# Optimization experiments

Measured on AMD Instinct MI355X. Metric: run time of the kernel, lower is better.

The kernel has to match this reference:

```python
import jax, jax.numpy as jnp
import numpy as np

N_HEADS = 16
ROPE_BASE = 10000.0


def setup_inputs() -> dict:
    key = jax.random.key(0)
    k1, k2, k3 = jax.random.split(key, 3)
    B, S, E = 8, 1024, 128
    sequence = jax.random.normal(k1, (B, S, E), dtype=jnp.float32)
    W_qkv = jax.random.normal(k2, (3 * N_HEADS * E, E), dtype=jnp.float32) * (E ** -0.5)
    b_qkv = jax.random.normal(k3, (3 * N_HEADS * E,), dtype=jnp.float32) * 0.02
    return {"sequence": sequence, "W_qkv": W_qkv, "b_qkv": b_qkv}


def _rope(x):
    # x: [B, H, S, D]; rotate-half (NeoX style) rotary encoding
    D = x.shape[-1]
    S = x.shape[-2]
    half = D // 2
    inv_freq = 1.0 / (ROPE_BASE ** (jnp.arange(0, half, dtype=jnp.float32) / half))
    angles = jnp.arange(S, dtype=jnp.float32)[:, None] * inv_freq[None, :]  # [S, half]
    cos = jnp.cos(angles)
    sin = jnp.sin(angles)
    x1, x2 = x[..., :half], x[..., half:]
    return jnp.concatenate([x1 * cos - x2 * sin, x1 * sin + x2 * cos], axis=-1)


def reference(sequence, W_qkv, b_qkv):
    B, S, E = sequence.shape
    H = N_HEADS
    # fused QKV projection: [B, S, 3*H*E]
    qkv = jnp.einsum('bse,fe->bsf', sequence, W_qkv) + b_qkv
    qkv = qkv.reshape(B, S, 3, H, E)
    # split and move head dim: [B, H, S, E]
    q = jnp.transpose(qkv[:, :, 0], (0, 2, 1, 3))
    k = jnp.transpose(qkv[:, :, 1], (0, 2, 1, 3))
    v = jnp.transpose(qkv[:, :, 2], (0, 2, 1, 3))
    q = _rope(q)
    k = _rope(k)
    # scaled dot-product attention (non-causal, dropout_p=0 for input layer)
    scale = 1.0 / jnp.sqrt(jnp.asarray(E, dtype=q.dtype))
    scores = jnp.einsum('bhqd,bhkd->bhqk', q, k) * scale
    probs = jax.nn.softmax(scores, axis=-1)
    attn = jnp.einsum('bhqk,bhkd->bhqd', probs, v)
    # back to [B, S, H, E]
    return jnp.transpose(attn, (0, 2, 1, 3))
```

## Files before the change

kernel.cpp:

```cpp
#include <hip/hip_runtime.h>
#include <hip/hip_bf16.h>
#include <math.h>

typedef __attribute__((ext_vector_type(8))) short bf16x8;
typedef __attribute__((ext_vector_type(4))) float f32x4;
typedef __attribute__((ext_vector_type(16))) float f32x16;

#define B_ 8
#define S_ 1024
#define E_ 128
#define H_ 16
#define M_ (B_*S_)
#define F_ (3*H_*E_)

__device__ __forceinline__ unsigned short f2b(float x) {
  __hip_bfloat16 h = __float2bfloat16(x);
  return *reinterpret_cast<unsigned short*>(&h);
}

__device__ __forceinline__ f32x4 mfma16(bf16x8 a, bf16x8 b, f32x4 c) {
  return __builtin_amdgcn_mfma_f32_16x16x32_bf16(a, b, c, 0, 0, 0);
}
__device__ __forceinline__ f32x16 mfma32(bf16x8 a, bf16x8 b, f32x16 c) {
  return __builtin_amdgcn_mfma_f32_32x32x16_bf16(a, b, c, 0, 0, 0);
}
__device__ __forceinline__ unsigned cvtpk(float a, float b) {
  unsigned r; asm("v_cvt_pk_bf16_f32 %0, %1, %2" : "=v"(r) : "v"(a), "v"(b)); return r;
}

__global__ __launch_bounds__(256) void prep_kernel(
    const float* __restrict__ seq, const float* __restrict__ wq,
    unsigned short* __restrict__ seqb, unsigned short* __restrict__ wb,
    float* __restrict__ ctab, float* __restrict__ stab)
{
  int i = blockIdx.x * 256 + threadIdx.x;
  if (i < M_*E_/4) {
    float4 v = reinterpret_cast<const float4*>(seq)[i];
    ushort4 o; o.x = f2b(v.x); o.y = f2b(v.y); o.z = f2b(v.z); o.w = f2b(v.w);
    reinterpret_cast<ushort4*>(seqb)[i] = o;
  }
  if (i < F_*E_/4) {
    float4 v = reinterpret_cast<const float4*>(wq)[i];
    ushort4 o; o.x = f2b(v.x); o.y = f2b(v.y); o.z = f2b(v.z); o.w = f2b(v.w);
    reinterpret_cast<ushort4*>(wb)[i] = o;
  }
  if (i < S_*64) {
    int s = i >> 6, e = i & 63;
    double ang = (double)s * pow(10000.0, -(double)e / 64.0);
    ctab[i] = (float)cos(ang);
    stab[i] = (float)sin(ang);
  }
}

__global__ __launch_bounds__(256) void qkv_gemm_kernel(
    const unsigned short* __restrict__ Ab, const unsigned short* __restrict__ Wb,
    const float* __restrict__ bias, const float* __restrict__ ctab, const float* __restrict__ stab,
    unsigned short* __restrict__ qo, unsigned short* __restrict__ ko, unsigned short* __restrict__ vt)
{
  __shared__ unsigned short As[128][136];
  __shared__ unsigned short Ws[128][136];
  const int bm = blockIdx.x, bn = blockIdx.y;
  const int t = threadIdx.x;
  const int w = t >> 6, l = t & 63, lc = l & 15, g = l >> 4;

  #pragma unroll
  for (int i = 0; i < 8; ++i) {
    int c = t + i * 256, row = c >> 4, kc = c & 15;
    *reinterpret_cast<bf16x8*>(&As[row][kc*8]) =
        *reinterpret_cast<const bf16x8*>(&Ab[(size_t)(bm*128+row)*128 + kc*8]);
    *reinterpret_cast<bf16x8*>(&Ws[row][kc*8]) =
        *reinterpret_cast<const bf16x8*>(&Wb[(size_t)(bn*128+row)*128 + kc*8]);
  }
  __syncthreads();

  const f32x4 zero = {0.f, 0.f, 0.f, 0.f};
  f32x4 acc[2][8];
  #pragma unroll
  for (int mi=0;mi<2;mi++)
    #pragma unroll
    for (int nj=0;nj<8;nj++) acc[mi][nj] = zero;

  #pragma unroll
  for (int ks = 0; ks < 4; ++ks) {
    bf16x8 a[2], b[8];
    #pragma unroll
    for (int mi=0;mi<2;mi++)
      a[mi] = *reinterpret_cast<const bf16x8*>(&As[w*32 + mi*16 + lc][ks*32 + g*8]);
    #pragma unroll
    for (int nj=0;nj<8;nj++)
      b[nj] = *reinterpret_cast<const bf16x8*>(&Ws[nj*16 + lc][ks*32 + g*8]);
    #pragma unroll
    for (int mi=0;mi<2;mi++)
      #pragma unroll
      for (int nj=0;nj<8;nj++)
        acc[mi][nj] = mfma16(a[mi], b[nj], acc[mi][nj]);
  }

  float bv[8];
  #pragma unroll
  for (int nj=0;nj<8;nj++) bv[nj] = bias[bn*128 + nj*16 + lc];

  const int c3 = bn >> 4, h = bn & 15;
  if (c3 < 2) {
    unsigned short* dst = (c3 == 0) ? qo : ko;
    const float mul = (c3 == 1) ? 0.12751742f : 1.0f;
    #pragma unroll
    for (int mi=0;mi<2;mi++)
      #pragma unroll
      for (int r=0;r<4;r++) {
        int mrow = bm*128 + w*32 + mi*16 + g*4 + r;
        int bb = mrow >> 10, s = mrow & 1023;
        size_t ob = ((size_t)(bb*H_ + h)*S_ + s)*E_;
        #pragma unroll
        for (int nj=0;nj<4;nj++) {
          int e1 = nj*16 + lc;
          float x1 = acc[mi][nj][r]   + bv[nj];
          float x2 = acc[mi][nj+4][r] + bv[nj+4];
          float cs = ctab[s*64 + e1], sn = stab[s*64 + e1];
          dst[ob + e1]      = f2b((x1*cs - x2*sn) * mul);
          dst[ob + e1 + 64] = f2b((x1*sn + x2*cs) * mul);
        }
      }
  } else {
    __syncthreads();
    const int gsw = ((g & 1) << 1) | (g >> 1);
    #pragma unroll
    for (int mi=0;mi<2;mi++)
      #pragma unroll
      for (int nj=0;nj<8;nj++)
        #pragma unroll
        for (int r=0;r<4;r++)
          As[nj*16 + lc][w*32 + mi*16 + gsw*4 + r] = f2b(acc[mi][nj][r] + bv[nj]);
    __syncthreads();
    int bb = bm >> 3, sb = (bm & 7) * 128;
    #pragma unroll
    for (int i=0;i<8;i++) {
      int cidx = t + i*256, e = cidx >> 4, sc = cidx & 15;
      *reinterpret_cast<bf16x8*>(&vt[((size_t)(bb*H_ + h)*E_ + e)*S_ + sb + sc*8]) =
          *reinterpret_cast<const bf16x8*>(&As[e][sc*8]);
    }
  }
}

__global__ __launch_bounds__(256, 2) void attn_kernel(
    const unsigned short* __restrict__ qg, const unsigned short* __restrict__ kg,
    const unsigned short* __restrict__ vtg, float* __restrict__ out)
{
  __shared__ unsigned short Ks[2][32*128];
  __shared__ unsigned short Vs[2][128*32];
  const int bh = blockIdx.x, qb = blockIdx.y;
  const int t = threadIdx.x, w = t >> 6, l = t & 63;
  const int q32 = l & 31, hi = l >> 5;
  const size_t base = (size_t)bh * (S_*E_);
  const int bb = bh >> 4, h = bh & 15;

  bf16x8 qreg[2][8];
  #pragma unroll
  for (int qb2=0;qb2<2;qb2++) {
    const unsigned short* qrow = qg + base + (size_t)(qb*256 + w*64 + qb2*32 + q32)*E_;
    #pragma unroll
    for (int dc=0;dc<8;dc++)
      qreg[qb2][dc] = *reinterpret_cast<const bf16x8*>(qrow + dc*16 + hi*8);
  }

  const char* kbase = (const char*)&Ks[0][0];
  const char* vbase = (const char*)&Vs[0][0];
  const char* kp[4];
  #pragma unroll
  for (int dc=0; dc<4; dc++)
    kp[dc] = kbase + q32*256 + (((dc*2 + hi) ^ q32) & 7) * 16;
  const char* vp[2];
  #pragma unroll
  for (int kb=0; kb<2; kb++)
    vp[kb] = vbase + q32*64 + (((kb*2 + hi) ^ (q32 >> 1)) & 3) * 16;

  const unsigned short* ksrc[2]; const unsigned short* vsrc[2];
  #pragma unroll
  for (int i=0;i<2;i++) {
    int idx = i*256 + t;
    int r = idx >> 4, cb = idx & 15;
    int sb = (cb & 8) | ((cb ^ r) & 7);
    ksrc[i] = kg + base + (size_t)r*E_ + sb*8;
    int rd = idx >> 2, vb = idx & 3;
    int svb = (vb ^ (rd >> 1)) & 3;
    vsrc[i] = vtg + base + (size_t)rd*S_ + svb*8;
  }

  auto stage = [&](int bufi, int tt) {
    #pragma unroll
    for (int i=0;i<2;i++)
      __builtin_amdgcn_global_load_lds(
        (const __attribute__((address_space(1))) void*)(ksrc[i] + (size_t)tt*32*E_),
        (__attribute__((address_space(3))) void*)(&Ks[bufi][(i*256 + w*64)*8]),
        16, 0, 0);
    #pragma unroll
    for (int i=0;i<2;i++)
      __builtin_amdgcn_global_load_lds(
        (const __attribute__((address_space(1))) void*)(vsrc[i] + (size_t)tt*32),
        (__attribute__((address_space(3))) void*)(&Vs[bufi][(i*256 + w*64)*8]),
        16, 0, 0);
  };

  const f32x16 z16 = {0,0,0,0,0,0,0,0,0,0,0,0,0,0,0,0};
  f32x16 accO[8];
  #pragma unroll
  for (int i=0;i<8;i++) accO[i] = z16;
  float lsum[2] = {0.f, 0.f};

  stage(0, 0);
  __syncthreads();

  #pragma unroll 2
  for (int tt = 0; tt < 32; ++tt) {
    const int cur = tt & 1;
    const int kOF = cur * 8192;
    const int vOF = cur * 8192;

    f32x16 s0 = z16, s1 = z16;
    __builtin_amdgcn_s_setprio(1);
    #pragma unroll
    for (int dc=0; dc<8; dc++) {
      bf16x8 kf = *reinterpret_cast<const bf16x8*>(kp[dc & 3] + ((dc & 4) ? 128 : 0) + kOF);
      s0 = mfma32(kf, qreg[0][dc], s0);
      s1 = mfma32(kf, qreg[1][dc], s1);
    }
    __builtin_amdgcn_s_setprio(0);

    if (tt < 31) stage(cur ^ 1, tt + 1);

    bf16x8 pu[2][2];
    #pragma unroll
    for (int qb2=0; qb2<2; qb2++) {
      f32x16& sv = qb2 ? s1 : s0;
      float sa0 = 0.f, sa1 = 0.f;
      #pragma unroll
      for (int kb=0; kb<2; kb++) {
        union { unsigned u[4]; bf16x8 v; } uu;
        #pragma unroll
        for (int c=0; c<4; c++) {
          float pa = __builtin_amdgcn_exp2f(sv[kb*8 + c*2]);
          float pb = __builtin_amdgcn_exp2f(sv[kb*8 + c*2 + 1]);
          sa0 += pa; sa1 += pb;
          uu.u[c] = cvtpk(pa, pb);
        }
        pu[qb2][kb] = uu.v;
      }
      lsum[qb2] += sa0 + sa1;
    }

    __builtin_amdgcn_s_setprio(1);
    #pragma unroll
    for (int dc=0; dc<4; dc++)
      #pragma unroll
      for (int kb=0; kb<2; kb++) {
        bf16x8 vf = *reinterpret_cast<const bf16x8*>(vp[kb] + dc*2048 + vOF);
        accO[dc]   = mfma32(vf, pu[0][kb], accO[dc]);
        accO[4+dc] = mfma32(vf, pu[1][kb], accO[4+dc]);
      }
    __builtin_amdgcn_s_setprio(0);

    __syncthreads();
  }

  #pragma unroll
  for (int qb2=0; qb2<2; qb2++) {
    float lt = lsum[qb2] + __shfl_xor(lsum[qb2], 32);
    float inv = 1.0f / lt;
    const int s = qb*256 + w*64 + qb2*32 + q32;
    float* orow = out + ((size_t)(bb*S_ + s)*H_ + h)*E_;
    #pragma unroll
    for (int dc=0;dc<4;dc++)
      #pragma unroll
      for (int rq=0;rq<4;rq++) {
        float4 o4;
        o4.x = accO[qb2*4+dc][rq*4+0]*inv;
        o4.y = accO[qb2*4+dc][rq*4+1]*inv;
        o4.z = accO[qb2*4+dc][rq*4+2]*inv;
        o4.w = accO[qb2*4+dc][rq*4+3]*inv;
        *reinterpret_cast<float4*>(orow + dc*32 + rq*8 + hi*4) = o4;
      }
  }
}

extern "C" void kernel_launch(void* const* d_in, const int* in_sizes, int n_in,
                              void* d_out, int out_size, void* d_ws, size_t ws_size,
                              hipStream_t stream) {
  const float* seq = (const float*)d_in[0];
  const float* wq  = (const float*)d_in[1];
  const float* bq  = (const float*)d_in[2];
  float* out = (float*)d_out;
  char* ws = (char*)d_ws;
  size_t off = 0;
  unsigned short* seqb = (unsigned short*)(ws + off); off += (size_t)M_*E_*2;
  unsigned short* wb   = (unsigned short*)(ws + off); off += (size_t)F_*E_*2;
  float* ctab = (float*)(ws + off); off += (size_t)S_*64*4;
  float* stab = (float*)(ws + off); off += (size_t)S_*64*4;
  unsigned short* qbuf = (unsigned short*)(ws + off); off += (size_t)B_*H_*S_*E_*2;
  unsigned short* kbuf = (unsigned short*)(ws + off); off += (size_t)B_*H_*S_*E_*2;
  unsigned short* vtbuf= (unsigned short*)(ws + off); off += (size_t)B_*H_*S_*E_*2;

  prep_kernel<<<dim3(1024), dim3(256), 0, stream>>>(seq, wq, seqb, wb, ctab, stab);
  qkv_gemm_kernel<<<dim3(64, 48), dim3(256), 0, stream>>>(seqb, wb, bq, ctab, stab, qbuf, kbuf, vtbuf);
  attn_kernel<<<dim3(128, 4), dim3(256), 0, stream>>>(qbuf, kbuf, vtbuf, out);
}
```

Baseline: 129.8 us.

## Software-pipeline attention loop with triple-buffered K/V and interleaved PV/QK MFMAs

Restructures the attention main loop so the P·V MFMAs for the previous tile are interleaved with the Q·K MFMAs for the current tile. K/V shared-memory staging goes from double to triple buffering, so the prefetch can run one tile further ahead. The softmax of tile t can then overlap with MFMA work from a neighbouring tile, and there is one barrier per iteration. It raises LDS use (48KB per block) and register pressure, which may reduce occupancy at launch_bounds(256,2).

```diff
diff --git a/kernel.cpp b/kernel.cpp
--- a/kernel.cpp
+++ b/kernel.cpp
@@ -146,8 +146,8 @@
     const unsigned short* __restrict__ qg, const unsigned short* __restrict__ kg,
     const unsigned short* __restrict__ vtg, float* __restrict__ out)
 {
-  __shared__ unsigned short Ks[2][32*128];
-  __shared__ unsigned short Vs[2][128*32];
+  __shared__ unsigned short Ks[3][32*128];
+  __shared__ unsigned short Vs[3][128*32];
   const int bh = blockIdx.x, qb = blockIdx.y;
   const int t = threadIdx.x, w = t >> 6, l = t & 63;
   const int q32 = l & 31, hi = l >> 5;
@@ -206,29 +206,9 @@
   #pragma unroll
   for (int i=0;i<8;i++) accO[i] = z16;
   float lsum[2] = {0.f, 0.f};
-
-  stage(0, 0);
-  __syncthreads();
-
-  #pragma unroll 2
-  for (int tt = 0; tt < 32; ++tt) {
-    const int cur = tt & 1;
-    const int kOF = cur * 8192;
-    const int vOF = cur * 8192;
-
-    f32x16 s0 = z16, s1 = z16;
-    __builtin_amdgcn_s_setprio(1);
-    #pragma unroll
-    for (int dc=0; dc<8; dc++) {
-      bf16x8 kf = *reinterpret_cast<const bf16x8*>(kp[dc & 3] + ((dc & 4) ? 128 : 0) + kOF);
-      s0 = mfma32(kf, qreg[0][dc], s0);
-      s1 = mfma32(kf, qreg[1][dc], s1);
-    }
-    __builtin_amdgcn_s_setprio(0);
-
-    if (tt < 31) stage(cur ^ 1, tt + 1);
-
-    bf16x8 pu[2][2];
+  bf16x8 pu[2][2];
+
+  auto softmax_pack = [&](f32x16& s0, f32x16& s1) {
     #pragma unroll
     for (int qb2=0; qb2<2; qb2++) {
       f32x16& sv = qb2 ? s1 : s0;
@@ -247,20 +227,61 @@
       }
       lsum[qb2] += sa0 + sa1;
     }
-
+  };
+
+  stage(0, 0);
+  __syncthreads();
+  {
+    f32x16 s0 = z16, s1 = z16;
+    stage(1, 1);
     __builtin_amdgcn_s_setprio(1);
     #pragma unroll
-    for (int dc=0; dc<4; dc++)
-      #pragma unroll
-      for (int kb=0; kb<2; kb++) {
-        bf16x8 vf = *reinterpret_cast<const bf16x8*>(vp[kb] + dc*2048 + vOF);
-        accO[dc]   = mfma32(vf, pu[0][kb], accO[dc]);
-        accO[4+dc] = mfma32(vf, pu[1][kb], accO[4+dc]);
-      }
+    for (int dc=0; dc<8; dc++) {
+      bf16x8 kf = *reinterpret_cast<const bf16x8*>(kp[dc & 3] + ((dc & 4) ? 128 : 0));
+      s0 = mfma32(kf, qreg[0][dc], s0);
+      s1 = mfma32(kf, qreg[1][dc], s1);
+    }
     __builtin_amdgcn_s_setprio(0);
-
-    __syncthreads();
-  }
+    softmax_pack(s0, s1);
+  }
+
+#define FUSED_BODY(PRV, CUR, T, DOSTAGE)                                          \
+  {                                                                               \
+    __syncthreads();                                                              \
+    if (DOSTAGE) stage(((CUR) + 1) % 3, (T) + 1);                                 \
+    f32x16 s0 = z16, s1 = z16;                                                    \
+    __builtin_amdgcn_s_setprio(1);                                                \
+    _Pragma("unroll")                                                             \
+    for (int i = 0; i < 8; ++i) {                                                 \
+      int dc_ = i, pd_ = i >> 1, pk_ = i & 1;                                     \
+      bf16x8 vf = *reinterpret_cast<const bf16x8*>(vp[pk_] + pd_*2048 + (PRV)*8192); \
+      accO[pd_]   = mfma32(vf, pu[0][pk_], accO[pd_]);                            \
+      accO[4+pd_] = mfma32(vf, pu[1][pk_], accO[4+pd_]);                          \
+      bf16x8 kf = *reinterpret_cast<const bf16x8*>(kp[dc_ & 3] + ((dc_ & 4) ? 128 : 0) + (CUR)*8192); \
+      s0 = mfma32(kf, qreg[0][dc_], s0);                                          \
+      s1 = mfma32(kf, qreg[1][dc_], s1);                                          \
+    }                                                                             \
+    __builtin_amdgcn_s_setprio(0);                                                \
+    softmax_pack(s0, s1);                                                         \
+  }
+
+  for (int j = 0; j < 10; ++j) {
+    FUSED_BODY(0, 1, 3*j + 1, true)
+    FUSED_BODY(1, 2, 3*j + 2, true)
+    FUSED_BODY(2, 0, 3*j + 3, (3*j + 3 < 31))
+  }
+  FUSED_BODY(0, 1, 31, false)
+
+  __builtin_amdgcn_s_setprio(1);
+  #pragma unroll
+  for (int i = 0; i < 8; ++i) {
+    int pd_ = i >> 1, pk_ = i & 1;
+    bf16x8 vf = *reinterpret_cast<const bf16x8*>(vp[pk_] + pd_*2048 + 1*8192);
+    accO[pd_]   = mfma32(vf, pu[0][pk_], accO[pd_]);
+    accO[4+pd_] = mfma32(vf, pu[1][pk_], accO[4+pd_]);
+  }
+  __builtin_amdgcn_s_setprio(0);
+#undef FUSED_BODY
 
   #pragma unroll
   for (int qb2=0; qb2<2; qb2++) {
```

New measurement: 162.9 us. +25.5%, slower.
